# Kernel tuning notes

Measured on AMD Instinct MI355X. Metric: run time of the kernel, lower is better.

Reference implementation:

```python
import jax, jax.numpy as jnp
import numpy as np

B, T, D, H = 8, 512, 768, 768
LN_EPS = 1e-3  # keras LayerNormalization default epsilon


def setup_inputs() -> dict:
    key = jax.random.key(0)
    ks = jax.random.split(key, 16)
    s = 1.0 / np.sqrt(D)  # glorot-ish scale for weight matrices
    return {
        'x': jax.random.normal(ks[0], (B, T, D), jnp.float32),
        'ln1_g': jnp.ones((D,), jnp.float32),
        'ln1_b': jnp.zeros((D,), jnp.float32),
        'ln2_g': jnp.ones((D,), jnp.float32),
        'ln2_b': jnp.zeros((D,), jnp.float32),
        'tm_mix_k': jax.random.uniform(ks[1], (D,), jnp.float32, 0.0, 2.0 / D),
        'tm_mix_v': jax.random.uniform(ks[2], (D,), jnp.float32, 0.0, 2.0 / D),
        'tm_mix_r': jax.random.uniform(ks[3], (D,), jnp.float32, 0.0, (2.0 / D) ** 0.5),
        'tm_key_w': jax.random.normal(ks[4], (D, H), jnp.float32) * s,
        'tm_value_w': jax.random.normal(ks[5], (D, H), jnp.float32) * s,
        'tm_rec_w': jax.random.normal(ks[6], (D, H), jnp.float32) * s,
        'time_decay': jax.random.uniform(ks[7], (H,), jnp.float32, 0.0, 1.0),
        'time_first': jax.random.uniform(ks[8], (H,), jnp.float32, 0.0, 0.05),
        'out_w': jax.random.normal(ks[9], (H, D), jnp.float32) * s,
        'cm_mix_k': jax.random.uniform(ks[10], (D,), jnp.float32, 0.0, 2.0 / D),
        'cm_mix_r': jax.random.uniform(ks[11], (D,), jnp.float32, 0.0, 2.0 / D),
        'cm_key_w': jax.random.normal(ks[12], (D, 4 * H), jnp.float32) * s,
        'cm_value_w': jax.random.normal(ks[13], (4 * H, D), jnp.float32) * (0.5 * s),
        'cm_rec_w': jax.random.normal(ks[14], (D, D), jnp.float32) * s,
    }


def _layernorm(z, g, b):
    m = jnp.mean(z, axis=-1, keepdims=True)
    v = jnp.var(z, axis=-1, keepdims=True)
    return (z - m) * jax.lax.rsqrt(v + LN_EPS) * g + b


def reference(x, ln1_g, ln1_b, ln2_g, ln2_b, tm_mix_k, tm_mix_v, tm_mix_r,
              tm_key_w, tm_value_w, tm_rec_w, time_decay, time_first, out_w,
              cm_mix_k, cm_mix_r, cm_key_w, cm_value_w, cm_rec_w):
    # x: [B, T, D]. Sequential RWKV WKV recurrence over T via lax.scan.
    def step(carry, x_t):
        s_cm, s_tm, num, den, q = carry  # [B,D],[B,D],[B,H],[B,H],[B,H]
        # ---- time mixing on ln_1(x_t) ----
        xi = _layernorm(x_t, ln1_g, ln1_b)
        xk = xi * tm_mix_k + s_tm * (1.0 - tm_mix_k)
        xv = xi * tm_mix_v + s_tm * (1.0 - tm_mix_v)
        xr = xi * tm_mix_r + s_tm * (1.0 - tm_mix_r)
        k = xk @ tm_key_w                      # [B,H]
        v = xv @ tm_value_w                    # [B,H]
        sr = jax.nn.sigmoid(xr @ tm_rec_w)     # [B,H]
        # max-stabilized wkv readout
        w = time_first + k
        qq = jnp.maximum(q, w)
        e1 = jnp.exp(q - qq)
        e2 = jnp.exp(w - qq)
        wkv = (e1 * num + e2 * v) / (e1 * den + e2)
        # state update with decay
        w2 = q - jnp.exp(time_decay)
        q_new = jnp.maximum(w2, k)
        e1 = jnp.exp(w2 - q_new)
        e2 = jnp.exp(k - q_new)
        num_new = e1 * num + e2 * v
        den_new = e1 * den + e2
        y = x_t + (sr * wkv) @ out_w
        # ---- channel mixing on ln_2(y) ----
        xc = _layernorm(y, ln2_g, ln2_b)
        xk2 = xc * cm_mix_k + s_cm * (1.0 - cm_mix_k)
        xr2 = xc * cm_mix_r + s_cm * (1.0 - cm_mix_r)
        kv = jnp.square(jax.nn.relu(xk2 @ cm_key_w)) @ cm_value_w
        y = y + jax.nn.sigmoid(xr2 @ cm_rec_w) * kv
        return (xc, xi, num_new, den_new, q_new), y

    b = x.shape[0]
    d = tm_key_w.shape[0]
    h = tm_key_w.shape[1]
    zD = jnp.zeros((b, d), x.dtype)
    zH = jnp.zeros((b, h), x.dtype)
    init = (zD, zD, zH, zH, zH)
    _, ys = jax.lax.scan(step, init, jnp.swapaxes(x, 0, 1))  # ys: [T,B,D]
    return jnp.swapaxes(ys, 0, 1)
```

## Files before the change

### kernel.cpp

```cpp
#include <hip/hip_runtime.h>
#include <cstdint>
#include <cstddef>

#define B_ 8
#define T_ 512
#define D_ 768
#define H_ 768
#define BT_ 4096
#define LN_EPS 1e-3f

typedef short bf16x8 __attribute__((ext_vector_type(8)));
typedef float f32x4 __attribute__((ext_vector_type(4)));

__device__ __forceinline__ ushort f2bf(float f) {
    union { float f; unsigned u; } x; x.f = f;
    unsigned r = (x.u + 0x7FFFu + ((x.u >> 16) & 1u)) >> 16;
    return (ushort)r;
}
__device__ __forceinline__ float bf2f(ushort u) {
    union { unsigned u; float f; } x; x.u = ((unsigned)u) << 16;
    return x.f;
}

#define GLOAD_LDS16(gp, lp)                                                        \
    __builtin_amdgcn_global_load_lds((const __attribute__((address_space(1))) void*)(gp), \
                                     (__attribute__((address_space(3))) void*)(lp), 16, 0, 0)

struct PrepArgs {
    const float *x, *g, *b, *mk, *mv, *mr;
    ushort *xk, *xv, *xr;
    const float* ws[7];
    ushort* wd[7];
};

__global__ __launch_bounds__(256) void prep(PrepArgs a) {
    __shared__ float tl[32][33];
    __shared__ float red[4][4];
    int bid = blockIdx.x;
    const int tid = threadIdx.x;
    if (bid < BT_) {
        const int row = bid;
        const int t = row & (T_ - 1);
        const float* xc = a.x + (size_t)row * D_;
        const float* xp = a.x + (size_t)(row - 1) * D_;
        const float c0 = xc[tid], c1 = xc[tid + 256], c2 = xc[tid + 512];
        float p0 = 0.f, p1 = 0.f, p2 = 0.f;
        if (t > 0) { p0 = xp[tid]; p1 = xp[tid + 256]; p2 = xp[tid + 512]; }
        float sc = c0 + c1 + c2, qc = c0 * c0 + c1 * c1 + c2 * c2;
        float sp = p0 + p1 + p2, qp = p0 * p0 + p1 * p1 + p2 * p2;
        #pragma unroll
        for (int off = 32; off > 0; off >>= 1) {
            sc += __shfl_down(sc, off); qc += __shfl_down(qc, off);
            sp += __shfl_down(sp, off); qp += __shfl_down(qp, off);
        }
        const int wid = tid >> 6;
        if ((tid & 63) == 0) { red[wid][0] = sc; red[wid][1] = qc; red[wid][2] = sp; red[wid][3] = qp; }
        __syncthreads();
        sc = red[0][0] + red[1][0] + red[2][0] + red[3][0];
        qc = red[0][1] + red[1][1] + red[2][1] + red[3][1];
        sp = red[0][2] + red[1][2] + red[2][2] + red[3][2];
        qp = red[0][3] + red[1][3] + red[2][3] + red[3][3];
        const float mc = sc * (1.0f / D_);
        const float rc = rsqrtf(qc * (1.0f / D_) - mc * mc + LN_EPS);
        const float mp = sp * (1.0f / D_);
        const float rp = rsqrtf(qp * (1.0f / D_) - mp * mp + LN_EPS);
        const size_t base = (size_t)row * D_;
        const float cv[3] = {c0, c1, c2};
        const float pv[3] = {p0, p1, p2};
        #pragma unroll
        for (int s = 0; s < 3; ++s) {
            const int d = tid + s * 256;
            const float cn = (cv[s] - mc) * rc * a.g[d] + a.b[d];
            const float pn = (t > 0) ? ((pv[s] - mp) * rp * a.g[d] + a.b[d]) : 0.0f;
            float m;
            m = a.mk[d]; a.xk[base + d] = f2bf(cn * m + pn * (1.f - m));
            m = a.mv[d]; a.xv[base + d] = f2bf(cn * m + pn * (1.f - m));
            m = a.mr[d]; a.xr[base + d] = f2bf(cn * m + pn * (1.f - m));
        }
        return;
    }
    bid -= BT_;
    int z, K, N, n0, k0;
    if (bid < 2880) {
        z = bid / 576; const int i = bid % 576;
        K = 768; N = 768; n0 = (i % 24) * 32; k0 = (i / 24) * 32;
    } else if (bid < 2880 + 2304) {
        z = 5; const int i = bid - 2880;
        K = 768; N = 3072; n0 = (i % 96) * 32; k0 = (i / 96) * 32;
    } else {
        z = 6; const int i = bid - 2880 - 2304;
        K = 3072; N = 768; n0 = (i % 24) * 32; k0 = (i / 24) * 32;
    }
    const float* W = a.ws[z];
    ushort* WT = a.wd[z];
    const int tx = tid & 31, ty = tid >> 5;
    #pragma unroll
    for (int i = 0; i < 4; ++i)
        tl[ty + i * 8][tx] = W[(size_t)(k0 + ty + i * 8) * N + n0 + tx];
    __syncthreads();
    #pragma unroll
    for (int i = 0; i < 4; ++i)
        WT[(size_t)(n0 + ty + i * 8) * K + k0 + tx] = f2bf(tl[tx][ty + i * 8]);
}

__global__ __launch_bounds__(256) void ln_cmix(const float* __restrict__ in,
                                               ushort* __restrict__ xk2,
                                               ushort* __restrict__ xr2,
                                               const float* __restrict__ g,
                                               const float* __restrict__ b,
                                               const float* __restrict__ mk,
                                               const float* __restrict__ mr) {
    const int row = blockIdx.x;
    const int t = row & (T_ - 1);
    const float* xc = in + (size_t)row * D_;
    const float* xp = in + (size_t)(row - 1) * D_;
    const int tid = threadIdx.x;
    const float c0 = xc[tid], c1 = xc[tid + 256], c2 = xc[tid + 512];
    float p0 = 0.f, p1 = 0.f, p2 = 0.f;
    if (t > 0) { p0 = xp[tid]; p1 = xp[tid + 256]; p2 = xp[tid + 512]; }
    float sc = c0 + c1 + c2, qc = c0 * c0 + c1 * c1 + c2 * c2;
    float sp = p0 + p1 + p2, qp = p0 * p0 + p1 * p1 + p2 * p2;
    #pragma unroll
    for (int off = 32; off > 0; off >>= 1) {
        sc += __shfl_down(sc, off); qc += __shfl_down(qc, off);
        sp += __shfl_down(sp, off); qp += __shfl_down(qp, off);
    }
    __shared__ float red[4][4];
    const int wid = tid >> 6;
    if ((tid & 63) == 0) { red[wid][0] = sc; red[wid][1] = qc; red[wid][2] = sp; red[wid][3] = qp; }
    __syncthreads();
    sc = red[0][0] + red[1][0] + red[2][0] + red[3][0];
    qc = red[0][1] + red[1][1] + red[2][1] + red[3][1];
    sp = red[0][2] + red[1][2] + red[2][2] + red[3][2];
    qp = red[0][3] + red[1][3] + red[2][3] + red[3][3];
    const float mc = sc * (1.0f / D_);
    const float rc = rsqrtf(qc * (1.0f / D_) - mc * mc + LN_EPS);
    const float mp = sp * (1.0f / D_);
    const float rp = rsqrtf(qp * (1.0f / D_) - mp * mp + LN_EPS);
    const size_t base = (size_t)row * D_;
    const float cv[3] = {c0, c1, c2};
    const float pv[3] = {p0, p1, p2};
    #pragma unroll
    for (int s = 0; s < 3; ++s) {
        const int d = tid + s * 256;
        const float cn = (cv[s] - mc) * rc * g[d] + b[d];
        const float pn = (t > 0) ? ((pv[s] - mp) * rp * g[d] + b[d]) : 0.0f;
        float m;
        m = mk[d]; xk2[base + d] = f2bf(cn * m + pn * (1.f - m));
        m = mr[d]; xr2[base + d] = f2bf(cn * m + pn * (1.f - m));
    }
}

#define WKV_CH 16
#define WKV_NC 16
#define WKV_L  32

__global__ __launch_bounds__(256) void wkv_scan(const ushort* __restrict__ k,
                                                const ushort* __restrict__ v,
                                                const ushort* __restrict__ srr,
                                                const float* __restrict__ time_decay,
                                                const float* __restrict__ time_first,
                                                ushort* __restrict__ rv) {
    const int c   = threadIdx.x & (WKV_CH - 1);
    const int ch  = threadIdx.x >> 4;
    const int gch = blockIdx.x * WKV_CH + c;
    const int b = gch / H_;
    const int h = gch % H_;
    const float ed = expf(time_decay[h]);
    const float tf = time_first[h];
    const size_t base = (size_t)b * T_ * H_ + h;

    float n = 0.f, d = 0.f, m = -1e30f;
    size_t idx = base + (size_t)(ch * WKV_L) * H_;
    #pragma unroll 4
    for (int t = 0; t < WKV_L; ++t, idx += H_) {
        const float kk = bf2f(k[idx]), vv = bf2f(v[idx]);
        const float w2 = m - ed;
        const float qn = fmaxf(w2, kk);
        const float e1 = expf(w2 - qn), e2 = expf(kk - qn);
        n = e1 * n + e2 * vv;
        d = e1 * d + e2;
        m = qn;
    }

    __shared__ float sn[WKV_NC][WKV_CH], sd[WKV_NC][WKV_CH], sm[WKV_NC][WKV_CH];
    sn[ch][c] = n; sd[ch][c] = d; sm[ch][c] = m;
    __syncthreads();

    if (ch == 0) {
        float pn = 0.f, pd = 0.f, pm = -1e30f;
        #pragma unroll
        for (int j = 0; j < WKV_NC; ++j) {
            const float nn = sn[j][c], dd = sd[j][c], m2 = sm[j][c];
            sn[j][c] = pn; sd[j][c] = pd; sm[j][c] = pm;
            const float w2 = pm - ed * (float)WKV_L;
            const float mm = fmaxf(w2, m2);
            const float e1 = expf(w2 - mm), e2 = expf(m2 - mm);
            pn = e1 * pn + e2 * nn;
            pd = e1 * pd + e2 * dd;
            pm = mm;
        }
    }
    __syncthreads();

    n = sn[ch][c]; d = sd[ch][c]; m = sm[ch][c];
    idx = base + (size_t)(ch * WKV_L) * H_;
    #pragma unroll 4
    for (int t = 0; t < WKV_L; ++t, idx += H_) {
        const float kk = bf2f(k[idx]), vv = bf2f(v[idx]), ss = bf2f(srr[idx]);
        const float w  = tf + kk;
        const float qq = fmaxf(m, w);
        const float e1 = expf(m - qq), e2 = expf(w - qq);
        const float wkvv = (e1 * n + e2 * vv) / (e1 * d + e2);
        rv[idx] = f2bf(ss * wkvv);
        const float w2 = m - ed;
        const float qn = fmaxf(w2, kk);
        const float a  = expf(w2 - qn), bb = expf(kk - qn);
        n = a * n + bb * vv;
        d = a * d + bb;
        m = qn;
    }
}

template <int BM, int NF>
__device__ __forceinline__ void run_gemm(const ushort* __restrict__ A,
                                         const ushort* __restrict__ Bt,
                                         int K, int bm, int bn,
                                         ushort* As, ushort* Bs,
                                         f32x4 (&acc)[BM / 32][NF], int t) {
    constexpr int MF = BM / 32;
    constexpr int BN = NF * 32;
    constexpr int ASTRIDE = BM * 64;
    constexpr int BSTRIDE = BN * 64;
    const int l = t & 63, wid = t >> 6;
    const int wr = wid >> 1, wc = wid & 1;
    const int lr = l & 15, lg = l >> 4;
    const int l8 = l >> 3, j8 = l & 7;
    const int gcol = ((j8 ^ l8) << 3);
    const int rsw = lr & 7;

    auto STAGE = [&](int buf, int k0) {
        #pragma unroll
        for (int p = 0; p < MF; ++p) {
            const int r = wid * (BM / 4) + p * 8 + l8;
            GLOAD_LDS16(A + (size_t)(bm + r) * K + k0 + gcol,
                        As + buf * ASTRIDE + (wid * (BM / 4) + p * 8) * 64);
        }
        #pragma unroll
        for (int p = 0; p < NF; ++p) {
            const int r = wid * (BN / 4) + p * 8 + l8;
            GLOAD_LDS16(Bt + (size_t)(bn + r) * K + k0 + gcol,
                        Bs + buf * BSTRIDE + (wid * (BN / 4) + p * 8) * 64);
        }
    };

    STAGE(0, 0);
    const int nt = K >> 6;
    int cur = 0;
    for (int it = 0; it < nt; ++it) {
        if (it + 1 < nt) {
            STAGE(cur ^ 1, (it + 1) << 6);
            constexpr int VC = MF + NF;
            if constexpr (VC == 4)      asm volatile("s_waitcnt vmcnt(4)" ::: "memory");
            else if constexpr (VC == 5) asm volatile("s_waitcnt vmcnt(5)" ::: "memory");
            else if constexpr (VC == 6) asm volatile("s_waitcnt vmcnt(6)" ::: "memory");
            else                        asm volatile("s_waitcnt vmcnt(8)" ::: "memory");
        } else {
            asm volatile("s_waitcnt vmcnt(0)" ::: "memory");
        }
        __builtin_amdgcn_sched_barrier(0);
        __builtin_amdgcn_s_barrier();
        const ushort* Ab = As + cur * ASTRIDE;
        const ushort* Bb = Bs + cur * BSTRIDE;
        #pragma unroll
        for (int ks = 0; ks < 2; ++ks) {
            const int cidx = ((ks * 4 + lg) ^ rsw) << 3;
            bf16x8 af[MF], bfr[NF];
            #pragma unroll
            for (int mf = 0; mf < MF; ++mf)
                af[mf] = *(const bf16x8*)(Ab + (wr * (BM / 2) + mf * 16 + lr) * 64 + cidx);
            #pragma unroll
            for (int nf = 0; nf < NF; ++nf)
                bfr[nf] = *(const bf16x8*)(Bb + (wc * (BN / 2) + nf * 16 + lr) * 64 + cidx);
            #pragma unroll
            for (int mf = 0; mf < MF; ++mf)
                #pragma unroll
                for (int nf = 0; nf < NF; ++nf)
                    acc[mf][nf] = __builtin_amdgcn_mfma_f32_16x16x32_bf16(
                        af[mf], bfr[nf], acc[mf][nf], 0, 0, 0);
        }
        __builtin_amdgcn_s_barrier();
        cur ^= 1;
    }
}

template <int BM, int NF>
__device__ __forceinline__ void run_gemm_sb(const ushort* __restrict__ A,
                                            const ushort* __restrict__ Bt,
                                            int K, int bm, int bn,
                                            ushort* As, ushort* Bs,
                                            f32x4 (&acc)[BM / 32][NF], int t) {
    constexpr int MF = BM / 32;
    constexpr int BN = NF * 32;
    constexpr int ASTRIDE = BM * 64;
    constexpr int BSTRIDE = BN * 64;
    const int l = t & 63, wid = t >> 6;
    const int wr = wid >> 1, wc = wid & 1;
    const int lr = l & 15, lg = l >> 4;
    const int l8 = l >> 3, j8 = l & 7;
    const int gcol = ((j8 ^ l8) << 3);
    const int rsw = lr & 7;

    auto STAGE = [&](int buf, int k0) {
        #pragma unroll
        for (int p = 0; p < MF; ++p) {
            const int r = wid * (BM / 4) + p * 8 + l8;
            GLOAD_LDS16(A + (size_t)(bm + r) * K + k0 + gcol,
                        As + buf * ASTRIDE + (wid * (BM / 4) + p * 8) * 64);
        }
        #pragma unroll
        for (int p = 0; p < NF; ++p) {
            const int r = wid * (BN / 4) + p * 8 + l8;
            GLOAD_LDS16(Bt + (size_t)(bn + r) * K + k0 + gcol,
                        Bs + buf * BSTRIDE + (wid * (BN / 4) + p * 8) * 64);
        }
    };

    STAGE(0, 0);
    const int nt = K >> 6;
    int cur = 0;
    for (int it = 0; it < nt; ++it) {
        if (it + 1 < nt) {
            int nb = cur + 1; if (nb == 3) nb = 0;
            STAGE(nb, (it + 1) << 6);
            constexpr int VC = MF + NF;
            if constexpr (VC == 4)      asm volatile("s_waitcnt vmcnt(4)" ::: "memory");
            else if constexpr (VC == 5) asm volatile("s_waitcnt vmcnt(5)" ::: "memory");
            else if constexpr (VC == 6) asm volatile("s_waitcnt vmcnt(6)" ::: "memory");
            else                        asm volatile("s_waitcnt vmcnt(8)" ::: "memory");
        } else {
            asm volatile("s_waitcnt vmcnt(0)" ::: "memory");
        }
        __builtin_amdgcn_sched_barrier(0);
        __builtin_amdgcn_s_barrier();
        __builtin_amdgcn_sched_barrier(0);
        const ushort* Ab = As + cur * ASTRIDE;
        const ushort* Bb = Bs + cur * BSTRIDE;
        #pragma unroll
        for (int ks = 0; ks < 2; ++ks) {
            const int cidx = ((ks * 4 + lg) ^ rsw) << 3;
            bf16x8 af[MF], bfr[NF];
            #pragma unroll
            for (int mf = 0; mf < MF; ++mf)
                af[mf] = *(const bf16x8*)(Ab + (wr * (BM / 2) + mf * 16 + lr) * 64 + cidx);
            #pragma unroll
            for (int nf = 0; nf < NF; ++nf)
                bfr[nf] = *(const bf16x8*)(Bb + (wc * (BN / 2) + nf * 16 + lr) * 64 + cidx);
            #pragma unroll
            for (int mf = 0; mf < MF; ++mf)
                #pragma unroll
                for (int nf = 0; nf < NF; ++nf)
                    acc[mf][nf] = __builtin_amdgcn_mfma_f32_16x16x32_bf16(
                        af[mf], bfr[nf], acc[mf][nf], 0, 0, 0);
        }
        cur += 1; if (cur == 3) cur = 0;
    }
}

enum { EPI_KVR = 0, EPI_ADDX = 1, EPI_RELU2 = 2 };

template <int EPI, int BM, int BN>
__global__ __launch_bounds__(256) void hgemm(const ushort* __restrict__ Abase,
                                             const ushort* __restrict__ Wbase,
                                             void* __restrict__ Cbase,
                                             const float* __restrict__ aux1,
                                             int M, int N, int K) {
    constexpr int NF = BN / 32;
    constexpr int MF = BM / 32;
    constexpr bool SB = (BN == 64);
    __shared__ ushort As[(SB ? 3 : 2) * BM * 64];
    __shared__ ushort Bs[(SB ? 3 : 2) * BN * 64];
    const int t = threadIdx.x;
    int lin = blockIdx.y * gridDim.x + blockIdx.x;
    const int q = (gridDim.x * gridDim.y) >> 3;
    lin = (lin & 7) * q + (lin >> 3);
    const int bn = (lin % gridDim.x) * BN;
    const int bm = (lin / gridDim.x) * BM;
    const int z = blockIdx.z;

    const ushort* A  = Abase;
    const ushort* Bt = Wbase;
    float*  Cf = (float*)Cbase;
    ushort* Cu = (ushort*)Cbase;
    if (EPI == EPI_KVR) {
        A  += (size_t)z * ((size_t)M * K);
        Bt += (size_t)z * ((size_t)N * K);
        Cu += (size_t)z * ((size_t)M * N);
    }

    f32x4 acc[MF][NF];
    #pragma unroll
    for (int i = 0; i < MF; ++i)
        #pragma unroll
        for (int j = 0; j < NF; ++j) acc[i][j] = (f32x4){0.f, 0.f, 0.f, 0.f};

    if constexpr (SB)
        run_gemm_sb<BM, NF>(A, Bt, K, bm, bn, As, Bs, acc, t);
    else
        run_gemm<BM, NF>(A, Bt, K, bm, bn, As, Bs, acc, t);

    const int l = t & 63, wid = t >> 6;
    const int wr = wid >> 1, wc = wid & 1;
    const int lr = l & 15, lg = l >> 4;
    #pragma unroll
    for (int mf = 0; mf < MF; ++mf) {
        #pragma unroll
        for (int nf = 0; nf < NF; ++nf) {
            const f32x4 a = acc[mf][nf];
            #pragma unroll
            for (int j = 0; j < 4; ++j) {
                const int row = bm + wr * (BM / 2) + mf * 16 + lg * 4 + j;
                const int col = bn + wc * (BN / 2) + nf * 16 + lr;
                const size_t idx = (size_t)row * N + col;
                const float vacc = a[j];
                if (EPI == EPI_KVR) {
                    Cu[idx] = f2bf((z == 2) ? 1.0f / (1.0f + expf(-vacc)) : vacc);
                } else if (EPI == EPI_ADDX) {
                    Cf[idx] = aux1[idx] + vacc;
                } else {
                    const float r = fmaxf(vacc, 0.0f);
                    Cu[idx] = f2bf(r * r);
                }
            }
        }
    }
}

__global__ __launch_bounds__(256) void kv_sigmul(const ushort* __restrict__ h1,
                                                 const ushort* __restrict__ wtCV,
                                                 const ushort* __restrict__ xr2,
                                                 const ushort* __restrict__ wtCR,
                                                 const float* __restrict__ ymid,
                                                 float* __restrict__ out) {
    __shared__ ushort As[3 * 64 * 64];
    __shared__ ushort Bs[3 * 64 * 64];
    const int t = threadIdx.x;
    int lin = blockIdx.y * gridDim.x + blockIdx.x;
    const int q = (gridDim.x * gridDim.y) >> 3;
    lin = (lin & 7) * q + (lin >> 3);
    const int bn = (lin % gridDim.x) * 64;
    const int bm = (lin / gridDim.x) * 64;

    f32x4 acc1[2][2], acc2[2][2];
    #pragma unroll
    for (int i = 0; i < 2; ++i)
        #pragma unroll
        for (int j = 0; j < 2; ++j) {
            acc1[i][j] = (f32x4){0.f, 0.f, 0.f, 0.f};
            acc2[i][j] = (f32x4){0.f, 0.f, 0.f, 0.f};
        }

    run_gemm_sb<64, 2>(h1, wtCV, 3072, bm, bn, As, Bs, acc1, t);
    __syncthreads();
    run_gemm_sb<64, 2>(xr2, wtCR, 768, bm, bn, As, Bs, acc2, t);

    const int l = t & 63, wid = t >> 6;
    const int wr = wid >> 1, wc = wid & 1;
    const int lr = l & 15, lg = l >> 4;
    #pragma unroll
    for (int mf = 0; mf < 2; ++mf) {
        #pragma unroll
        for (int nf = 0; nf < 2; ++nf) {
            #pragma unroll
            for (int j = 0; j < 4; ++j) {
                const int row = bm + wr * 32 + mf * 16 + lg * 4 + j;
                const int col = bn + wc * 32 + nf * 16 + lr;
                const size_t idx = (size_t)row * D_ + col;
                const float sig = 1.0f / (1.0f + expf(-acc2[mf][nf][j]));
                out[idx] = ymid[idx] + sig * acc1[mf][nf][j];
            }
        }
    }
}

extern "C" void kernel_launch(void* const* d_in, const int* in_sizes, int n_in,
                              void* d_out, int out_size, void* d_ws, size_t ws_size,
                              hipStream_t stream) {
    const float* x          = (const float*)d_in[0];
    const float* ln1_g      = (const float*)d_in[1];
    const float* ln1_b      = (const float*)d_in[2];
    const float* ln2_g      = (const float*)d_in[3];
    const float* ln2_b      = (const float*)d_in[4];
    const float* tm_mix_k   = (const float*)d_in[5];
    const float* tm_mix_v   = (const float*)d_in[6];
    const float* tm_mix_r   = (const float*)d_in[7];
    const float* tm_key_w   = (const float*)d_in[8];
    const float* tm_value_w = (const float*)d_in[9];
    const float* tm_rec_w   = (const float*)d_in[10];
    const float* time_decay = (const float*)d_in[11];
    const float* time_first = (const float*)d_in[12];
    const float* out_w      = (const float*)d_in[13];
    const float* cm_mix_k   = (const float*)d_in[14];
    const float* cm_mix_r   = (const float*)d_in[15];
    const float* cm_key_w   = (const float*)d_in[16];
    const float* cm_value_w = (const float*)d_in[17];
    const float* cm_rec_w   = (const float*)d_in[18];
    float* out = (float*)d_out;

    const size_t SZ = (size_t)BT_ * D_;
    float* wsf = (float*)d_ws;
    float* ymid = wsf;
    ushort* ub = (ushort*)(wsf + SZ);
    ushort* a0 = ub;
    ushort* a1 = ub + SZ;
    ushort* a2 = ub + 2 * SZ;
    ushort* h1 = ub + 3 * SZ;
    ushort* kvsr = ub + 7 * SZ;
    ushort* wt = ub + 10 * SZ;
    const size_t W66  = (size_t)768 * 768;
    const size_t WBIG = (size_t)768 * 3072;
    ushort* wtK  = wt;
    ushort* wtV  = wt + W66;
    ushort* wtR  = wt + 2 * W66;
    ushort* wtO  = wt + 3 * W66;
    ushort* wtCR = wt + 4 * W66;
    ushort* wtCK = wt + 5 * W66;
    ushort* wtCV = wt + 5 * W66 + WBIG;

    PrepArgs pa;
    pa.x = x; pa.g = ln1_g; pa.b = ln1_b;
    pa.mk = tm_mix_k; pa.mv = tm_mix_v; pa.mr = tm_mix_r;
    pa.xk = a0; pa.xv = a1; pa.xr = a2;
    pa.ws[0] = tm_key_w;   pa.wd[0] = wtK;
    pa.ws[1] = tm_value_w; pa.wd[1] = wtV;
    pa.ws[2] = tm_rec_w;   pa.wd[2] = wtR;
    pa.ws[3] = out_w;      pa.wd[3] = wtO;
    pa.ws[4] = cm_rec_w;   pa.wd[4] = wtCR;
    pa.ws[5] = cm_key_w;   pa.wd[5] = wtCK;
    pa.ws[6] = cm_value_w; pa.wd[6] = wtCV;

    prep<<<BT_ + 2880 + 2304 + 2304, 256, 0, stream>>>(pa);
    hgemm<EPI_KVR, 64, 64><<<dim3(12, 64, 3), 256, 0, stream>>>(a0, wtK, kvsr, nullptr, BT_, 768, 768);
    wkv_scan<<<(B_ * H_) / WKV_CH, 256, 0, stream>>>(kvsr, kvsr + SZ, kvsr + 2 * SZ,
                                                     time_decay, time_first, a0);
    hgemm<EPI_ADDX, 64, 64><<<dim3(12, 64), 256, 0, stream>>>(a0, wtO, ymid, x, BT_, 768, 768);
    ln_cmix<<<BT_, 256, 0, stream>>>(ymid, a1, a2, ln2_g, ln2_b, cm_mix_k, cm_mix_r);
    hgemm<EPI_RELU2, 64, 128><<<dim3(24, 64), 256, 0, stream>>>(a1, wtCK, h1, nullptr, BT_, 3072, 768);
    kv_sigmul<<<dim3(12, 64), 256, 0, stream>>>(h1, wtCV, a2, wtCR, ymid, out);
}
```

Baseline: 160.0 us.

## Split K across warp pairs in 64x64 GEMMs with LDS reduction

The 64x64 GEMM kernels (the KVR, ADDX and kv_sigmul paths) now give each warp the full 64-row M extent for one 32-wide K half of every 64-wide K step. Partial sums are then combined through LDS in a kreduce step. This halves the number of LDS B-fragment reads per MFMA and lets each warp issue 8 MFMAs per k-tile. The cost is more accumulator registers (occupancy hint of 3 blocks), extra barriers, and an LDS exchange at the end. The generic hgemm is trimmed to serve only the RELU2 path, with double buffering.

Result: slower. 311.9 us (+94.9%).

```diff
diff --git a/kernel.cpp b/kernel.cpp
--- a/kernel.cpp
+++ b/kernel.cpp
@@ -294,29 +294,30 @@
     }
 }
 
-template <int BM, int NF>
-__device__ __forceinline__ void run_gemm_sb(const ushort* __restrict__ A,
+template <int NF>
+__device__ __forceinline__ void run_gemm_ks(const ushort* __restrict__ A,
                                             const ushort* __restrict__ Bt,
                                             int K, int bm, int bn,
                                             ushort* As, ushort* Bs,
-                                            f32x4 (&acc)[BM / 32][NF], int t) {
-    constexpr int MF = BM / 32;
+                                            f32x4 (&acc)[4][NF], int t) {
+    constexpr int BM = 64;
     constexpr int BN = NF * 32;
     constexpr int ASTRIDE = BM * 64;
     constexpr int BSTRIDE = BN * 64;
     const int l = t & 63, wid = t >> 6;
-    const int wr = wid >> 1, wc = wid & 1;
+    const int wc = wid & 1, kh = wid >> 1;
     const int lr = l & 15, lg = l >> 4;
     const int l8 = l >> 3, j8 = l & 7;
     const int gcol = ((j8 ^ l8) << 3);
     const int rsw = lr & 7;
+    const int cidx = ((kh * 4 + lg) ^ rsw) << 3;
 
     auto STAGE = [&](int buf, int k0) {
         #pragma unroll
-        for (int p = 0; p < MF; ++p) {
-            const int r = wid * (BM / 4) + p * 8 + l8;
+        for (int p = 0; p < 2; ++p) {
+            const int r = wid * 16 + p * 8 + l8;
             GLOAD_LDS16(A + (size_t)(bm + r) * K + k0 + gcol,
-                        As + buf * ASTRIDE + (wid * (BM / 4) + p * 8) * 64);
+                        As + buf * ASTRIDE + (wid * 16 + p * 8) * 64);
         }
         #pragma unroll
         for (int p = 0; p < NF; ++p) {
@@ -333,11 +334,7 @@
         if (it + 1 < nt) {
             int nb = cur + 1; if (nb == 3) nb = 0;
             STAGE(nb, (it + 1) << 6);
-            constexpr int VC = MF + NF;
-            if constexpr (VC == 4)      asm volatile("s_waitcnt vmcnt(4)" ::: "memory");
-            else if constexpr (VC == 5) asm volatile("s_waitcnt vmcnt(5)" ::: "memory");
-            else if constexpr (VC == 6) asm volatile("s_waitcnt vmcnt(6)" ::: "memory");
-            else                        asm volatile("s_waitcnt vmcnt(8)" ::: "memory");
+            asm volatile("s_waitcnt vmcnt(4)" ::: "memory");
         } else {
             asm volatile("s_waitcnt vmcnt(0)" ::: "memory");
         }
@@ -346,28 +343,105 @@
         __builtin_amdgcn_sched_barrier(0);
         const ushort* Ab = As + cur * ASTRIDE;
         const ushort* Bb = Bs + cur * BSTRIDE;
-        #pragma unroll
-        for (int ks = 0; ks < 2; ++ks) {
-            const int cidx = ((ks * 4 + lg) ^ rsw) << 3;
-            bf16x8 af[MF], bfr[NF];
-            #pragma unroll
-            for (int mf = 0; mf < MF; ++mf)
-                af[mf] = *(const bf16x8*)(Ab + (wr * (BM / 2) + mf * 16 + lr) * 64 + cidx);
+        bf16x8 af[4], bfr[NF];
+        #pragma unroll
+        for (int mf = 0; mf < 4; ++mf)
+            af[mf] = *(const bf16x8*)(Ab + (mf * 16 + lr) * 64 + cidx);
+        #pragma unroll
+        for (int nf = 0; nf < NF; ++nf)
+            bfr[nf] = *(const bf16x8*)(Bb + (wc * 32 + nf * 16 + lr) * 64 + cidx);
+        #pragma unroll
+        for (int mf = 0; mf < 4; ++mf)
             #pragma unroll
             for (int nf = 0; nf < NF; ++nf)
-                bfr[nf] = *(const bf16x8*)(Bb + (wc * (BN / 2) + nf * 16 + lr) * 64 + cidx);
+                acc[mf][nf] = __builtin_amdgcn_mfma_f32_16x16x32_bf16(
+                    af[mf], bfr[nf], acc[mf][nf], 0, 0, 0);
+        cur += 1; if (cur == 3) cur = 0;
+    }
+}
+
+template <int NF>
+__device__ __forceinline__ void kreduce(f32x4 (&acc)[4][NF], ushort* scratch, int t) {
+    const int l = t & 63, wid = t >> 6;
+    const int kh = wid >> 1;
+    f32x4* xch = (f32x4*)scratch;
+    __syncthreads();
+    f32x4* w = xch + wid * (2 * NF * 64);
+    #pragma unroll
+    for (int mf = 0; mf < 2; ++mf)
+        #pragma unroll
+        for (int nf = 0; nf < NF; ++nf)
+            w[(mf * NF + nf) * 64 + l] = acc[2 * (kh ^ 1) + mf][nf];
+    __syncthreads();
+    const f32x4* r = xch + (wid ^ 2) * (2 * NF * 64);
+    #pragma unroll
+    for (int mf = 0; mf < 2; ++mf)
+        #pragma unroll
+        for (int nf = 0; nf < NF; ++nf)
+            acc[2 * kh + mf][nf] += r[(mf * NF + nf) * 64 + l];
+    __syncthreads();
+}
+
+enum { EPI_KVR = 0, EPI_ADDX = 1, EPI_RELU2 = 2 };
+
+template <int EPI>
+__global__ __launch_bounds__(256, 3) void hgemm_ks(const ushort* __restrict__ Abase,
+                                                   const ushort* __restrict__ Wbase,
+                                                   void* __restrict__ Cbase,
+                                                   const float* __restrict__ aux1,
+                                                   int M, int N, int K) {
+    __shared__ __align__(16) ushort As[3 * 64 * 64];
+    __shared__ __align__(16) ushort Bs[3 * 64 * 64];
+    const int t = threadIdx.x;
+    int lin = blockIdx.y * gridDim.x + blockIdx.x;
+    const int q = (gridDim.x * gridDim.y) >> 3;
+    lin = (lin & 7) * q + (lin >> 3);
+    const int bn = (lin % gridDim.x) * 64;
+    const int bm = (lin / gridDim.x) * 64;
+    const int z = blockIdx.z;
+
+    const ushort* A  = Abase;
+    const ushort* Bt = Wbase;
+    float*  Cf = (float*)Cbase;
+    ushort* Cu = (ushort*)Cbase;
+    if (EPI == EPI_KVR) {
+        A  += (size_t)z * ((size_t)M * K);
+        Bt += (size_t)z * ((size_t)N * K);
+        Cu += (size_t)z * ((size_t)M * N);
+    }
+
+    f32x4 acc[4][2];
+    #pragma unroll
+    for (int i = 0; i < 4; ++i)
+        #pragma unroll
+        for (int j = 0; j < 2; ++j) acc[i][j] = (f32x4){0.f, 0.f, 0.f, 0.f};
+
+    run_gemm_ks<2>(A, Bt, K, bm, bn, As, Bs, acc, t);
+    kreduce<2>(acc, As, t);
+
+    const int l = t & 63, wid = t >> 6;
+    const int wc = wid & 1, kh = wid >> 1;
+    const int lr = l & 15, lg = l >> 4;
+    #pragma unroll
+    for (int mf = 0; mf < 2; ++mf) {
+        #pragma unroll
+        for (int nf = 0; nf < 2; ++nf) {
+            const f32x4 a = acc[2 * kh + mf][nf];
             #pragma unroll
-            for (int mf = 0; mf < MF; ++mf)
-                #pragma unroll
-                for (int nf = 0; nf < NF; ++nf)
-                    acc[mf][nf] = __builtin_amdgcn_mfma_f32_16x16x32_bf16(
-                        af[mf], bfr[nf], acc[mf][nf], 0, 0, 0);
-        }
-        cur += 1; if (cur == 3) cur = 0;
-    }
-}
-
-enum { EPI_KVR = 0, EPI_ADDX = 1, EPI_RELU2 = 2 };
+            for (int j = 0; j < 4; ++j) {
+                const int row = bm + (2 * kh + mf) * 16 + lg * 4 + j;
+                const int col = bn + wc * 32 + nf * 16 + lr;
+                const size_t idx = (size_t)row * N + col;
+                const float vacc = a[j];
+                if (EPI == EPI_KVR) {
+                    Cu[idx] = f2bf((z == 2) ? 1.0f / (1.0f + expf(-vacc)) : vacc);
+                } else {
+                    Cf[idx] = aux1[idx] + vacc;
+                }
+            }
+        }
+    }
+}
 
 template <int EPI, int BM, int BN>
 __global__ __launch_bounds__(256) void hgemm(const ushort* __restrict__ Abase,
@@ -377,38 +451,24 @@
                                              int M, int N, int K) {
     constexpr int NF = BN / 32;
     constexpr int MF = BM / 32;
-    constexpr bool SB = (BN == 64);
-    __shared__ ushort As[(SB ? 3 : 2) * BM * 64];
-    __shared__ ushort Bs[(SB ? 3 : 2) * BN * 64];
+    __shared__ __align__(16) ushort As[2 * BM * 64];
+    __shared__ __align__(16) ushort Bs[2 * BN * 64];
     const int t = threadIdx.x;
     int lin = blockIdx.y * gridDim.x + blockIdx.x;
     const int q = (gridDim.x * gridDim.y) >> 3;
     lin = (lin & 7) * q + (lin >> 3);
     const int bn = (lin % gridDim.x) * BN;
     const int bm = (lin / gridDim.x) * BM;
-    const int z = blockIdx.z;
-
-    const ushort* A  = Abase;
-    const ushort* Bt = Wbase;
-    float*  Cf = (float*)Cbase;
+
+    f32x4 acc[MF][NF];
+    #pragma unroll
+    for (int i = 0; i < MF; ++i)
+        #pragma unroll
+        for (int j = 0; j < NF; ++j) acc[i][j] = (f32x4){0.f, 0.f, 0.f, 0.f};
+
+    run_gemm<BM, NF>(Abase, Wbase, K, bm, bn, As, Bs, acc, t);
+
     ushort* Cu = (ushort*)Cbase;
-    if (EPI == EPI_KVR) {
-        A  += (size_t)z * ((size_t)M * K);
-        Bt += (size_t)z * ((size_t)N * K);
-        Cu += (size_t)z * ((size_t)M * N);
-    }
-
-    f32x4 acc[MF][NF];
-    #pragma unroll
-    for (int i = 0; i < MF; ++i)
-        #pragma unroll
-        for (int j = 0; j < NF; ++j) acc[i][j] = (f32x4){0.f, 0.f, 0.f, 0.f};
-
-    if constexpr (SB)
-        run_gemm_sb<BM, NF>(A, Bt, K, bm, bn, As, Bs, acc, t);
-    else
-        run_gemm<BM, NF>(A, Bt, K, bm, bn, As, Bs, acc, t);
-
     const int l = t & 63, wid = t >> 6;
     const int wr = wid >> 1, wc = wid & 1;
     const int lr = l & 15, lg = l >> 4;
@@ -422,28 +482,21 @@
                 const int row = bm + wr * (BM / 2) + mf * 16 + lg * 4 + j;
                 const int col = bn + wc * (BN / 2) + nf * 16 + lr;
                 const size_t idx = (size_t)row * N + col;
-                const float vacc = a[j];
-                if (EPI == EPI_KVR) {
-                    Cu[idx] = f2bf((z == 2) ? 1.0f / (1.0f + expf(-vacc)) : vacc);
-                } else if (EPI == EPI_ADDX) {
-                    Cf[idx] = aux1[idx] + vacc;
-                } else {
-                    const float r = fmaxf(vacc, 0.0f);
-                    Cu[idx] = f2bf(r * r);
-                }
+                const float r = fmaxf(a[j], 0.0f);
+                Cu[idx] = f2bf(r * r);
             }
         }
     }
 }
 
-__global__ __launch_bounds__(256) void kv_sigmul(const ushort* __restrict__ h1,
-                                                 const ushort* __restrict__ wtCV,
-                                                 const ushort* __restrict__ xr2,
-                                                 const ushort* __restrict__ wtCR,
-                                                 const float* __restrict__ ymid,
-                                                 float* __restrict__ out) {
-    __shared__ ushort As[3 * 64 * 64];
-    __shared__ ushort Bs[3 * 64 * 64];
+__global__ __launch_bounds__(256, 3) void kv_sigmul(const ushort* __restrict__ h1,
+                                                    const ushort* __restrict__ wtCV,
+                                                    const ushort* __restrict__ xr2,
+                                                    const ushort* __restrict__ wtCR,
+                                                    const float* __restrict__ ymid,
+                                                    float* __restrict__ out) {
+    __shared__ __align__(16) ushort As[3 * 64 * 64];
+    __shared__ __align__(16) ushort Bs[3 * 64 * 64];
     const int t = threadIdx.x;
     int lin = blockIdx.y * gridDim.x + blockIdx.x;
     const int q = (gridDim.x * gridDim.y) >> 3;
@@ -451,21 +504,22 @@
     const int bn = (lin % gridDim.x) * 64;
     const int bm = (lin / gridDim.x) * 64;
 
-    f32x4 acc1[2][2], acc2[2][2];
-    #pragma unroll
-    for (int i = 0; i < 2; ++i)
+    f32x4 acc1[4][2], acc2[4][2];
+    #pragma unroll
+    for (int i = 0; i < 4; ++i)
         #pragma unroll
         for (int j = 0; j < 2; ++j) {
             acc1[i][j] = (f32x4){0.f, 0.f, 0.f, 0.f};
             acc2[i][j] = (f32x4){0.f, 0.f, 0.f, 0.f};
         }
 
-    run_gemm_sb<64, 2>(h1, wtCV, 3072, bm, bn, As, Bs, acc1, t);
-    __syncthreads();
-    run_gemm_sb<64, 2>(xr2, wtCR, 768, bm, bn, As, Bs, acc2, t);
+    run_gemm_ks<2>(h1, wtCV, 3072, bm, bn, As, Bs, acc1, t);
+    kreduce<2>(acc1, As, t);
+    run_gemm_ks<2>(xr2, wtCR, 768, bm, bn, As, Bs, acc2, t);
+    kreduce<2>(acc2, As, t);
 
     const int l = t & 63, wid = t >> 6;
-    const int wr = wid >> 1, wc = wid & 1;
+    const int wc = wid & 1, kh = wid >> 1;
     const int lr = l & 15, lg = l >> 4;
     #pragma unroll
     for (int mf = 0; mf < 2; ++mf) {
@@ -473,11 +527,11 @@
         for (int nf = 0; nf < 2; ++nf) {
             #pragma unroll
             for (int j = 0; j < 4; ++j) {
-                const int row = bm + wr * 32 + mf * 16 + lg * 4 + j;
+                const int row = bm + (2 * kh + mf) * 16 + lg * 4 + j;
                 const int col = bn + wc * 32 + nf * 16 + lr;
                 const size_t idx = (size_t)row * D_ + col;
-                const float sig = 1.0f / (1.0f + expf(-acc2[mf][nf][j]));
-                out[idx] = ymid[idx] + sig * acc1[mf][nf][j];
+                const float sig = 1.0f / (1.0f + expf(-acc2[2 * kh + mf][nf][j]));
+                out[idx] = ymid[idx] + sig * acc1[2 * kh + mf][nf][j];
             }
         }
     }
@@ -540,10 +594,10 @@
     pa.ws[6] = cm_value_w; pa.wd[6] = wtCV;
 
     prep<<<BT_ + 2880 + 2304 + 2304, 256, 0, stream>>>(pa);
-    hgemm<EPI_KVR, 64, 64><<<dim3(12, 64, 3), 256, 0, stream>>>(a0, wtK, kvsr, nullptr, BT_, 768, 768);
+    hgemm_ks<EPI_KVR><<<dim3(12, 64, 3), 256, 0, stream>>>(a0, wtK, kvsr, nullptr, BT_, 768, 768);
     wkv_scan<<<(B_ * H_) / WKV_CH, 256, 0, stream>>>(kvsr, kvsr + SZ, kvsr + 2 * SZ,
                                                      time_decay, time_first, a0);
-    hgemm<EPI_ADDX, 64, 64><<<dim3(12, 64), 256, 0, stream>>>(a0, wtO, ymid, x, BT_, 768, 768);
+    hgemm_ks<EPI_ADDX><<<dim3(12, 64), 256, 0, stream>>>(a0, wtO, ymid, x, BT_, 768, 768);
     ln_cmix<<<BT_, 256, 0, stream>>>(ymid, a1, a2, ln2_g, ln2_b, cm_mix_k, cm_mix_r);
     hgemm<EPI_RELU2, 64, 128><<<dim3(24, 64), 256, 0, stream>>>(a1, wtCK, h1, nullptr, BT_, 3072, 768);
     kv_sigmul<<<dim3(12, 64), 256, 0, stream>>>(h1, wtCV, a2, wtCR, ymid, out);
```
